# Performance work log

Hardware: AMD Instinct MI355X
Metric: run time of the kernel (lower is better)

## Reference

```python
import jax, jax.numpy as jnp
import numpy as np

FEATURE_MAP = 1024
DIM = 1024
SEQ_LEN = 128
BATCH = 128
WINDOW = 5


def setup_inputs() -> dict:
    key = jax.random.key(0)
    k1, k2 = jax.random.split(key)
    x = jax.random.normal(k1, (BATCH, SEQ_LEN, DIM), dtype=jnp.float32)
    # xavier-uniform-ish scale for Ws
    limit = np.sqrt(6.0 / (DIM + FEATURE_MAP)).astype(np.float32)
    Ws = jax.random.uniform(k2, (WINDOW, DIM, FEATURE_MAP), dtype=jnp.float32,
                            minval=-limit, maxval=limit)
    b = jnp.zeros((FEATURE_MAP,), dtype=jnp.float32)
    return {"x": x, "Ws": Ws, "b": b}


def reference(x, Ws, b):
    # x: [B, L, D] batch-first -> work in time-major order like the original.
    # Precompute all 5 projections for every timestep in one big einsum:
    # proj: [L, W, B, F]
    proj = jnp.einsum('bld,wdf->lwbf', x, Ws)
    B = x.shape[0]
    h0 = jnp.zeros((WINDOW, B, FEATURE_MAP), dtype=x.dtype)

    def step(h, p):
        # h, p: [W, B, F]
        # m1 = max(p0, h1); m_k = max(h_{k-1} + p_k, h_k) for k>=2 (old h used)
        cand = jnp.concatenate([p[:1], h[:-1] + p[1:]], axis=0)
        new_h = jnp.maximum(cand, h)
        return new_h, None

    h_final, _ = jax.lax.scan(step, h0, proj)
    return jnp.tanh(h_final[WINDOW - 1] + b[None, :])  # [B, F]
```

## Files before the change

### kernel.cpp

```cpp
#include <hip/hip_runtime.h>
#include <hip/hip_bf16.h>

#define WINDOW 5
#define DIM 1024
#define FEAT 1024
#define SEQ 128
#define BATCH 128
#define MTOT (BATCH*SEQ)
#define NTOT (WINDOW*FEAT)
#define KTOT 1024

#define DCHUNK 16

typedef int int4v __attribute__((ext_vector_type(4)));

static __device__ __forceinline__ unsigned short f2bf(float f) {
  union { float f; unsigned int i; } c; c.f = f;
  unsigned int i = c.i;
  unsigned int lsb = (i >> 16) & 1u;
  i += 0x7fffu + lsb;
  return (unsigned short)(i >> 16);
}
static __device__ __forceinline__ float bf2f(unsigned short u) {
  union { unsigned int i; float f; } c; c.i = ((unsigned int)u) << 16; return c.f;
}
static __device__ __forceinline__ signed char q8(float v, float inv) {
  float q = rintf(v * inv);
  q = fminf(fmaxf(q, -127.f), 127.f);
  return (signed char)(int)q;
}

__global__ __launch_bounds__(256) void quant_x(const float* __restrict__ x,
                                               signed char* __restrict__ xq,
                                               float* __restrict__ sx) {
  int row  = blockIdx.x * 4 + (threadIdx.x >> 6);
  int lane = threadIdx.x & 63;
  const float* xr = x + (size_t)row * KTOT;

  float4 v[4];
  float amax = 0.f;
  #pragma unroll
  for (int i = 0; i < 4; i++) {
    v[i] = ((const float4*)xr)[i * 64 + lane];
    amax = fmaxf(amax, fmaxf(fmaxf(fabsf(v[i].x), fabsf(v[i].y)),
                             fmaxf(fabsf(v[i].z), fabsf(v[i].w))));
  }
  #pragma unroll
  for (int m = 1; m < 64; m <<= 1)
    amax = fmaxf(amax, __shfl_xor(amax, m));

  float inv = amax > 0.f ? 127.f / amax : 0.f;
  int* xqr = (int*)(xq + (size_t)row * KTOT);
  #pragma unroll
  for (int i = 0; i < 4; i++) {
    int p = ((int)(unsigned char)q8(v[i].x, inv)) |
            ((int)(unsigned char)q8(v[i].y, inv) << 8) |
            ((int)(unsigned char)q8(v[i].z, inv) << 16) |
            ((int)q8(v[i].w, inv) << 24);
    xqr[i * 64 + lane] = p;
  }
  if (lane == 0) sx[row] = amax / 127.f;
}

__global__ __launch_bounds__(256) void w_colamax_part(const float* __restrict__ Ws,
                                                      float* __restrict__ part) {
  int w  = blockIdx.z;
  int dc = blockIdx.y;
  int f4 = threadIdx.x;
  const float* p = Ws + ((size_t)w * DIM + (size_t)dc * DCHUNK) * FEAT;
  float4 m = {0.f, 0.f, 0.f, 0.f};
  #pragma unroll
  for (int d = 0; d < DCHUNK; d++) {
    float4 v = ((const float4*)(p + (size_t)d * FEAT))[f4];
    m.x = fmaxf(m.x, fabsf(v.x));
    m.y = fmaxf(m.y, fabsf(v.y));
    m.z = fmaxf(m.z, fabsf(v.z));
    m.w = fmaxf(m.w, fabsf(v.w));
  }
  ((float4*)(part + ((size_t)w * (DIM / DCHUNK) + dc) * FEAT))[f4] = m;
}

__global__ __launch_bounds__(256) void w_colamax_reduce(const float* __restrict__ part,
                                                        float* __restrict__ sw) {
  int idx = blockIdx.x * 256 + threadIdx.x;
  int w = idx >> 10, f = idx & 1023;
  const float* p = part + (size_t)w * (DIM / DCHUNK) * FEAT + f;
  float m = 0.f;
  #pragma unroll 8
  for (int c = 0; c < DIM / DCHUNK; c++)
    m = fmaxf(m, p[(size_t)c * FEAT]);
  sw[idx] = m / 127.f;
}

__global__ __launch_bounds__(256) void transq_ws(const float* __restrict__ Ws,
                                                 const float* __restrict__ sw,
                                                 signed char* __restrict__ wq) {
  __shared__ float tile[32][33];
  int w  = blockIdx.z;
  int f0 = blockIdx.x * 32, d0 = blockIdx.y * 32;
  int tx = threadIdx.x, ty = threadIdx.y;
  const float* src = Ws + ((size_t)w * DIM + d0) * FEAT + f0;
  #pragma unroll
  for (int i = 0; i < 4; i++)
    tile[ty + 8*i][tx] = src[(size_t)(ty + 8*i) * FEAT + tx];
  __syncthreads();
  signed char* dst = wq + ((size_t)w * FEAT + f0) * DIM + d0;
  #pragma unroll
  for (int i = 0; i < 4; i++) {
    int f = f0 + ty + 8*i;
    float swv = sw[(w << 10) + f];
    float inv = swv > 0.f ? 1.0f / swv : 0.f;
    dst[(size_t)(ty + 8*i) * DIM + tx] = q8(tile[tx][ty + 8*i], inv);
  }
}

__global__ __launch_bounds__(256, 3) void fused_gemm_scan(
    const signed char* __restrict__ xq,
    const signed char* __restrict__ wq,
    const float* __restrict__ sx,
    const float* __restrict__ swp,
    const float* __restrict__ bias,
    float* __restrict__ out)
{
  __shared__ __align__(16) char smem[40960];
  signed char* As = (signed char*)smem;
  signed char* Bs = (signed char*)(smem + 16384);

  const int tid  = threadIdx.x;
  const int wid  = tid >> 6;
  const int lane = tid & 63;

  int bid = blockIdx.x;
  int wg  = ((bid & 7) << 9) + (bid >> 3);
  const int b  = wg >> 5;
  const int f0 = (wg & 31) << 5;

  const signed char* aG = xq + (size_t)b * SEQ * KTOT;

  const int wm = wid >> 1, wn = wid & 1;
  const int rowin = lane >> 3;
  const int swb16 = ((lane & 7) ^ rowin) << 4;

  int4v acc[4][5];
  #pragma unroll
  for (int i = 0; i < 4; i++)
    #pragma unroll
    for (int j = 0; j < 5; j++)
      acc[i][j] = (int4v){0, 0, 0, 0};

  for (int kt = 0; kt < 8; kt++) {
    const int k0 = kt << 7;
    #pragma unroll
    for (int c = 0; c < 9; c++) {
      int seg = wid * 9 + c;
      if (seg < 16) {
        int row = (seg << 3) + rowin;
        __builtin_amdgcn_global_load_lds(
            (const __attribute__((address_space(1))) void*)(aG + (size_t)row * KTOT + k0 + swb16),
            (__attribute__((address_space(3))) void*)(As + (seg << 10)), 16, 0, 0);
      } else {
        int sb = seg - 16;
        int r  = (sb << 3) + rowin;
        const signed char* src = wq
            + ((size_t)(((r >> 5) << 10) + f0 + (r & 31))) * KTOT + k0 + swb16;
        __builtin_amdgcn_global_load_lds(
            (const __attribute__((address_space(1))) void*)src,
            (__attribute__((address_space(3))) void*)(Bs + (sb << 10)), 16, 0, 0);
      }
    }
    __syncthreads();

    #pragma unroll
    for (int kk = 0; kk < 2; kk++) {
      int4v a[4], bf[5];
      #pragma unroll
      for (int i = 0; i < 4; i++) {
        int row  = wm * 64 + i * 16 + (lane & 15);
        int slot = (lane >> 4) + (kk << 2);
        a[i] = *(const int4v*)(As + row * 128 + ((slot ^ (row & 7)) << 4));
      }
      #pragma unroll
      for (int j = 0; j < 5; j++) {
        int row  = wn * 80 + j * 16 + (lane & 15);
        int slot = (lane >> 4) + (kk << 2);
        bf[j] = *(const int4v*)(Bs + row * 128 + ((slot ^ (row & 7)) << 4));
      }
      #pragma unroll
      for (int i = 0; i < 4; i++)
        #pragma unroll
        for (int j = 0; j < 5; j++)
          acc[i][j] = __builtin_amdgcn_mfma_i32_16x16x64_i8(a[i], bf[j], acc[i][j], 0, 0, 0);
    }
    __syncthreads();
  }

  float sxv[16];
  #pragma unroll
  for (int i = 0; i < 4; i++)
    #pragma unroll
    for (int r = 0; r < 4; r++)
      sxv[i * 4 + r] = sx[b * SEQ + wm * 64 + i * 16 + ((lane >> 4) << 2) + r];
  float swv[5];
  #pragma unroll
  for (int j = 0; j < 5; j++) {
    int c = wn * 80 + j * 16 + (lane & 15);
    swv[j] = swp[((c >> 5) << 10) + f0 + (c & 31)];
  }

  #pragma unroll
  for (int i = 0; i < 4; i++) {
    #pragma unroll
    for (int j = 0; j < 5; j++) {
      #pragma unroll
      for (int r = 0; r < 4; r++) {
        int l = wm * 64 + i * 16 + ((lane >> 4) << 2) + r;
        int c = wn * 80 + j * 16 + (lane & 15);
        float v = (float)acc[i][j][r] * sxv[i * 4 + r] * swv[j];
        int byte = ((l * 160 + c) << 1) ^ (((l >> 2) & 3) << 5);
        *(unsigned short*)(smem + byte) = f2bf(v);
      }
    }
  }
  __syncthreads();

  if (tid < 32) {
    const int f = tid;
    float h0 = 0.f, h1 = 0.f, h2 = 0.f, h3 = 0.f, h4 = 0.f;
    for (int l = 0; l < SEQ; l++) {
      const int swz  = ((l >> 2) & 3) << 5;
      const int base = l * 320;
      float p[5];
      #pragma unroll
      for (int w = 0; w < 5; w++) {
        int byte = (base + (((w << 5) + f) << 1)) ^ swz;
        p[w] = bf2f(*(const unsigned short*)(smem + byte));
      }
      h4 = fmaxf(h3 + p[4], h4);
      h3 = fmaxf(h2 + p[3], h3);
      h2 = fmaxf(h1 + p[2], h2);
      h1 = fmaxf(h0 + p[1], h1);
      h0 = fmaxf(p[0], h0);
    }
    out[b * FEAT + f0 + f] = tanhf(h4 + bias[f0 + f]);
  }
}

extern "C" void kernel_launch(void* const* d_in, const int* in_sizes, int n_in,
                              void* d_out, int out_size, void* d_ws, size_t ws_size,
                              hipStream_t stream) {
  const float* x  = (const float*)d_in[0];
  const float* Ws = (const float*)d_in[1];
  const float* b  = (const float*)d_in[2];
  float* out = (float*)d_out;

  char* ws = (char*)d_ws;
  const size_t XQ_BYTES = (size_t)MTOT * KTOT;
  const size_t WQ_BYTES = (size_t)WINDOW * FEAT * DIM;
  const size_t SX_BYTES = (size_t)MTOT * 4;
  const size_t SW_BYTES = (size_t)WINDOW * FEAT * 4;
  signed char* xq = (signed char*)ws;
  signed char* wq = (signed char*)(ws + XQ_BYTES);
  float* sx   = (float*)(ws + XQ_BYTES + WQ_BYTES);
  float* sw   = (float*)(ws + XQ_BYTES + WQ_BYTES + SX_BYTES);
  float* part = (float*)(ws + XQ_BYTES + WQ_BYTES + SX_BYTES + SW_BYTES);

  hipLaunchKernelGGL(quant_x, dim3(MTOT / 4), dim3(256), 0, stream, x, xq, sx);
  hipLaunchKernelGGL(w_colamax_part, dim3(1, DIM / DCHUNK, WINDOW), dim3(256), 0, stream,
                     Ws, part);
  hipLaunchKernelGGL(w_colamax_reduce, dim3(NTOT / 256), dim3(256), 0, stream, part, sw);
  hipLaunchKernelGGL(transq_ws, dim3(FEAT / 32, DIM / 32, WINDOW), dim3(32, 8), 0, stream,
                     Ws, sw, wq);
  hipLaunchKernelGGL(fused_gemm_scan, dim3(BATCH * 32), dim3(256), 0, stream,
                     xq, wq, sx, sw, b, out);
}
```

Measured before the change: 175.4 us.

## Pre-tile int8 operands into MFMA fragment layout and load directly to registers

The quantization kernels now write x and Ws in a fragment-major tiled layout, so each lane's 16-byte MFMA operand sits contiguously per 16x64 tile. The GEMM drops LDS staging and its barriers, loads fragments straight from global memory into registers, and double-buffers even/odd k-slices in software. Occupancy hint drops from 3 to 2 blocks per CU to make room for the extra registers. Operand reuse across waves now depends on the L1/L2 caches rather than shared memory, which may raise global traffic. The transpose-quantize kernel also moves to 64x64 tiles with float4 reads.

```diff
diff --git a/kernel.cpp b/kernel.cpp
--- a/kernel.cpp
+++ b/kernel.cpp
@@ -31,7 +31,7 @@
 }
 
 __global__ __launch_bounds__(256) void quant_x(const float* __restrict__ x,
-                                               signed char* __restrict__ xq,
+                                               signed char* __restrict__ xqf,
                                                float* __restrict__ sx) {
   int row  = blockIdx.x * 4 + (threadIdx.x >> 6);
   int lane = threadIdx.x & 63;
@@ -50,14 +50,17 @@
     amax = fmaxf(amax, __shfl_xor(amax, m));
 
   float inv = amax > 0.f ? 127.f / amax : 0.f;
-  int* xqr = (int*)(xq + (size_t)row * KTOT);
+  const int mtile = row >> 4, mr = row & 15;
   #pragma unroll
   for (int i = 0; i < 4; i++) {
     int p = ((int)(unsigned char)q8(v[i].x, inv)) |
             ((int)(unsigned char)q8(v[i].y, inv) << 8) |
             ((int)(unsigned char)q8(v[i].z, inv) << 16) |
             ((int)q8(v[i].w, inv) << 24);
-    xqr[i * 64 + lane] = p;
+    int k = i * 256 + lane * 4;
+    size_t addr = ((size_t)(mtile * 16 + (k >> 6))) * 1024
+                + (size_t)((mr + 16 * ((k >> 4) & 3)) * 16 + (k & 15));
+    *(int*)(xqf + addr) = p;
   }
   if (lane == 0) sx[row] = amax / 127.f;
 }
@@ -94,37 +97,53 @@
 
 __global__ __launch_bounds__(256) void transq_ws(const float* __restrict__ Ws,
                                                  const float* __restrict__ sw,
-                                                 signed char* __restrict__ wq) {
-  __shared__ float tile[32][33];
+                                                 signed char* __restrict__ wqf) {
+  __shared__ float tile[64][65];
   int w  = blockIdx.z;
-  int f0 = blockIdx.x * 32, d0 = blockIdx.y * 32;
-  int tx = threadIdx.x, ty = threadIdx.y;
-  const float* src = Ws + ((size_t)w * DIM + d0) * FEAT + f0;
-  #pragma unroll
-  for (int i = 0; i < 4; i++)
-    tile[ty + 8*i][tx] = src[(size_t)(ty + 8*i) * FEAT + tx];
+  int f0 = blockIdx.x * 64, d0 = blockIdx.y * 64;
+  int t  = threadIdx.x;
+  {
+    int drow = t >> 4, ff4 = (t & 15) * 4;
+    const float* src = Ws + ((size_t)w * DIM + d0) * FEAT + f0;
+    #pragma unroll
+    for (int p = 0; p < 4; p++) {
+      int d = p * 16 + drow;
+      float4 v = *(const float4*)(src + (size_t)d * FEAT + ff4);
+      tile[d][ff4]     = v.x;
+      tile[d][ff4 + 1] = v.y;
+      tile[d][ff4 + 2] = v.z;
+      tile[d][ff4 + 3] = v.w;
+    }
+  }
   __syncthreads();
-  signed char* dst = wq + ((size_t)w * FEAT + f0) * DIM + d0;
-  #pragma unroll
-  for (int i = 0; i < 4; i++) {
-    int f = f0 + ty + 8*i;
-    float swv = sw[(w << 10) + f];
+  {
+    int fl = t & 63, ks = t >> 6;
+    float swv = sw[(w << 10) + f0 + fl];
     float inv = swv > 0.f ? 1.0f / swv : 0.f;
-    dst[(size_t)(ty + 8*i) * DIM + tx] = q8(tile[tx][ty + 8*i], inv);
-  }
-}
-
-__global__ __launch_bounds__(256, 3) void fused_gemm_scan(
-    const signed char* __restrict__ xq,
-    const signed char* __restrict__ wq,
+    unsigned int pk[4];
+    #pragma unroll
+    for (int g = 0; g < 4; g++) {
+      unsigned int acc = 0;
+      #pragma unroll
+      for (int e = 0; e < 4; e++)
+        acc |= ((unsigned int)(unsigned char)q8(tile[ks * 16 + g * 4 + e][fl], inv)) << (8 * e);
+      pk[g] = acc;
+    }
+    size_t addr = ((size_t)((w * 64 + ((f0 + fl) >> 4)) * 16 + (d0 >> 6))) * 1024
+                + (size_t)(((fl & 15) + 16 * ks) * 16);
+    *(int4v*)(wqf + addr) = (int4v){(int)pk[0], (int)pk[1], (int)pk[2], (int)pk[3]};
+  }
+}
+
+__global__ __launch_bounds__(256, 2) void fused_gemm_scan(
+    const signed char* __restrict__ xqf,
+    const signed char* __restrict__ wqf,
     const float* __restrict__ sx,
     const float* __restrict__ swp,
     const float* __restrict__ bias,
     float* __restrict__ out)
 {
   __shared__ __align__(16) char smem[40960];
-  signed char* As = (signed char*)smem;
-  signed char* Bs = (signed char*)(smem + 16384);
 
   const int tid  = threadIdx.x;
   const int wid  = tid >> 6;
@@ -135,11 +154,21 @@
   const int b  = wg >> 5;
   const int f0 = (wg & 31) << 5;
 
-  const signed char* aG = xq + (size_t)b * SEQ * KTOT;
-
   const int wm = wid >> 1, wn = wid & 1;
-  const int rowin = lane >> 3;
-  const int swb16 = ((lane & 7) ^ rowin) << 4;
+
+  const signed char* aB[4];
+  #pragma unroll
+  for (int i = 0; i < 4; i++) {
+    int mt = b * 8 + wm * 4 + i;
+    aB[i] = xqf + (size_t)mt * 16384 + lane * 16;
+  }
+  const signed char* bB[5];
+  #pragma unroll
+  for (int j = 0; j < 5; j++) {
+    int c  = wn * 80 + j * 16;
+    int tl = (c >> 5) * 64 + (f0 >> 4) + ((c >> 4) & 1);
+    bB[j] = wqf + (size_t)tl * 16384 + lane * 16;
+  }
 
   int4v acc[4][5];
   #pragma unroll
@@ -148,50 +177,42 @@
     for (int j = 0; j < 5; j++)
       acc[i][j] = (int4v){0, 0, 0, 0};
 
-  for (int kt = 0; kt < 8; kt++) {
-    const int k0 = kt << 7;
-    #pragma unroll
-    for (int c = 0; c < 9; c++) {
-      int seg = wid * 9 + c;
-      if (seg < 16) {
-        int row = (seg << 3) + rowin;
-        __builtin_amdgcn_global_load_lds(
-            (const __attribute__((address_space(1))) void*)(aG + (size_t)row * KTOT + k0 + swb16),
-            (__attribute__((address_space(3))) void*)(As + (seg << 10)), 16, 0, 0);
-      } else {
-        int sb = seg - 16;
-        int r  = (sb << 3) + rowin;
-        const signed char* src = wq
-            + ((size_t)(((r >> 5) << 10) + f0 + (r & 31))) * KTOT + k0 + swb16;
-        __builtin_amdgcn_global_load_lds(
-            (const __attribute__((address_space(1))) void*)src,
-            (__attribute__((address_space(3))) void*)(Bs + (sb << 10)), 16, 0, 0);
-      }
-    }
-    __syncthreads();
-
-    #pragma unroll
-    for (int kk = 0; kk < 2; kk++) {
-      int4v a[4], bf[5];
-      #pragma unroll
-      for (int i = 0; i < 4; i++) {
-        int row  = wm * 64 + i * 16 + (lane & 15);
-        int slot = (lane >> 4) + (kk << 2);
-        a[i] = *(const int4v*)(As + row * 128 + ((slot ^ (row & 7)) << 4));
-      }
-      #pragma unroll
-      for (int j = 0; j < 5; j++) {
-        int row  = wn * 80 + j * 16 + (lane & 15);
-        int slot = (lane >> 4) + (kk << 2);
-        bf[j] = *(const int4v*)(Bs + row * 128 + ((slot ^ (row & 7)) << 4));
-      }
-      #pragma unroll
-      for (int i = 0; i < 4; i++)
-        #pragma unroll
-        for (int j = 0; j < 5; j++)
-          acc[i][j] = __builtin_amdgcn_mfma_i32_16x16x64_i8(a[i], bf[j], acc[i][j], 0, 0, 0);
-    }
-    __syncthreads();
+  int4v aE[4], bE[5], aO[4], bO[5];
+  #pragma unroll
+  for (int i = 0; i < 4; i++) aE[i] = *(const int4v*)(aB[i]);
+  #pragma unroll
+  for (int j = 0; j < 5; j++) bE[j] = *(const int4v*)(bB[j]);
+
+  #pragma unroll
+  for (int sb = 0; sb < 8; sb++) {
+    const int se = sb * 2;
+    #pragma unroll
+    for (int i = 0; i < 4; i++) aO[i] = *(const int4v*)(aB[i] + (se & 3) * 1024 + 1024);
+    #pragma unroll
+    for (int j = 0; j < 5; j++) bO[j] = *(const int4v*)(bB[j] + (se & 3) * 1024 + 1024);
+    #pragma unroll
+    for (int i = 0; i < 4; i++)
+      #pragma unroll
+      for (int j = 0; j < 5; j++)
+        acc[i][j] = __builtin_amdgcn_mfma_i32_16x16x64_i8(aE[i], bE[j], acc[i][j], 0, 0, 0);
+    if ((se & 3) == 2) {
+      #pragma unroll
+      for (int i = 0; i < 4; i++) aB[i] += 4096;
+      #pragma unroll
+      for (int j = 0; j < 5; j++) bB[j] += 4096;
+    }
+    if (sb < 7) {
+      const int nse = se + 2;
+      #pragma unroll
+      for (int i = 0; i < 4; i++) aE[i] = *(const int4v*)(aB[i] + (nse & 3) * 1024);
+      #pragma unroll
+      for (int j = 0; j < 5; j++) bE[j] = *(const int4v*)(bB[j] + (nse & 3) * 1024);
+    }
+    #pragma unroll
+    for (int i = 0; i < 4; i++)
+      #pragma unroll
+      for (int j = 0; j < 5; j++)
+        acc[i][j] = __builtin_amdgcn_mfma_i32_16x16x64_i8(aO[i], bO[j], acc[i][j], 0, 0, 0);
   }
 
   float sxv[16];
@@ -258,18 +279,18 @@
   const size_t WQ_BYTES = (size_t)WINDOW * FEAT * DIM;
   const size_t SX_BYTES = (size_t)MTOT * 4;
   const size_t SW_BYTES = (size_t)WINDOW * FEAT * 4;
-  signed char* xq = (signed char*)ws;
-  signed char* wq = (signed char*)(ws + XQ_BYTES);
+  signed char* xqf = (signed char*)ws;
+  signed char* wqf = (signed char*)(ws + XQ_BYTES);
   float* sx   = (float*)(ws + XQ_BYTES + WQ_BYTES);
   float* sw   = (float*)(ws + XQ_BYTES + WQ_BYTES + SX_BYTES);
   float* part = (float*)(ws + XQ_BYTES + WQ_BYTES + SX_BYTES + SW_BYTES);
 
-  hipLaunchKernelGGL(quant_x, dim3(MTOT / 4), dim3(256), 0, stream, x, xq, sx);
+  hipLaunchKernelGGL(quant_x, dim3(MTOT / 4), dim3(256), 0, stream, x, xqf, sx);
   hipLaunchKernelGGL(w_colamax_part, dim3(1, DIM / DCHUNK, WINDOW), dim3(256), 0, stream,
                      Ws, part);
   hipLaunchKernelGGL(w_colamax_reduce, dim3(NTOT / 256), dim3(256), 0, stream, part, sw);
-  hipLaunchKernelGGL(transq_ws, dim3(FEAT / 32, DIM / 32, WINDOW), dim3(32, 8), 0, stream,
-                     Ws, sw, wq);
+  hipLaunchKernelGGL(transq_ws, dim3(FEAT / 64, DIM / 64, WINDOW), dim3(256), 0, stream,
+                     Ws, sw, wqf);
   hipLaunchKernelGGL(fused_gemm_scan, dim3(BATCH * 32), dim3(256), 0, stream,
-                     xq, wq, sx, sw, b, out);
-}
+                     xqf, wqf, sx, sw, b, out);
+}
```

Result: slower. 282.9 us (+61.2%).
